# Performance work log

Hardware: AMD Instinct MI355X
Metric: run time of the kernel (lower is better)

The kernel has to match this reference:

```python
import jax, jax.numpy as jnp
import numpy as np

XYZ_MIN = jnp.array([-1.0, -1.0, -1.0], dtype=jnp.float32)
XYZ_MAX = jnp.array([1.0, 1.0, 1.0], dtype=jnp.float32)
ACT_SHIFT = float(np.log(1.0 / (1.0 - 1e-6) - 1.0))  # density bias shift
WS = 100  # world_size per axis for num_voxels=1024000 in [-1,1]^3
R, P = 4096, 128  # rays, points per ray


def grid_sample_3d(grid, xyz):
    """Trilinear grid_sample, align_corners=True, zeros padding.
    grid: [C, D, H, W] (D=z, H=y, W=x); xyz: [N, 3] world coords. Returns [N, C]."""
    C, D, H, W = grid.shape
    norm = (xyz - XYZ_MIN) / (XYZ_MAX - XYZ_MIN) * 2.0 - 1.0  # [-1,1]
    sizes = jnp.array([W, H, D], dtype=norm.dtype)
    pix = (norm + 1.0) * 0.5 * (sizes - 1.0)  # align_corners=True mapping
    p0f = jnp.floor(pix)
    frac = pix - p0f
    p0 = p0f.astype(jnp.int32)
    out = jnp.zeros((xyz.shape[0], C), dtype=grid.dtype)
    for dx in (0, 1):
        for dy in (0, 1):
            for dz in (0, 1):
                ix, iy, iz = p0[:, 0] + dx, p0[:, 1] + dy, p0[:, 2] + dz
                wx = frac[:, 0] if dx else 1.0 - frac[:, 0]
                wy = frac[:, 1] if dy else 1.0 - frac[:, 1]
                wz = frac[:, 2] if dz else 1.0 - frac[:, 2]
                valid = ((ix >= 0) & (ix < W) & (iy >= 0) & (iy < H)
                         & (iz >= 0) & (iz < D))
                ixc = jnp.clip(ix, 0, W - 1)
                iyc = jnp.clip(iy, 0, H - 1)
                izc = jnp.clip(iz, 0, D - 1)
                vals = grid[:, izc, iyc, ixc].T  # [N, C]
                out = out + vals * (wx * wy * wz * valid)[:, None]
    return out


def setup_inputs() -> dict:
    key = jax.random.key(0)
    ks = jax.random.split(key, 12)
    origins = jax.random.uniform(ks[0], (R, 3), jnp.float32, -0.5, 0.5)
    directions = jax.random.normal(ks[1], (R, 3), jnp.float32)
    lengths = jax.random.uniform(ks[2], (R, P), jnp.float32, 0.05, 0.6)
    grid_density = jax.random.normal(ks[3], (1, WS, WS, WS), jnp.float32) * 0.1
    grid_color = jax.random.normal(ks[4], (12, WS, WS, WS), jnp.float32) * 0.1
    d_in = 12 + 27
    w1 = jax.random.normal(ks[5], (d_in, 128), jnp.float32) / np.sqrt(d_in)
    b1 = jnp.zeros((128,), jnp.float32)
    w2 = jax.random.normal(ks[6], (128, 128), jnp.float32) / np.sqrt(128)
    b2 = jnp.zeros((128,), jnp.float32)
    w3 = jax.random.normal(ks[7], (128, 3), jnp.float32) / np.sqrt(128)
    b3 = jnp.zeros((3,), jnp.float32)
    return dict(origins=origins, directions=directions, lengths=lengths,
                grid_density=grid_density, grid_color=grid_color,
                w1=w1, b1=b1, w2=w2, b2=b2, w3=w3, b3=b3)


def reference(origins, directions, lengths, grid_density, grid_color,
              w1, b1, w2, b2, w3, b3):
    # ray points: [R, P, 3]
    pts = origins[:, None, :] + directions[:, None, :] * lengths[:, :, None]
    flat = pts.reshape(-1, 3)
    # density branch
    density = grid_sample_3d(grid_density, flat).reshape(R, P, 1)
    interval = jnp.linalg.norm(directions, axis=-1)[:, None, None]
    alpha = 1.0 - (1.0 + jnp.exp(density + ACT_SHIFT)) ** (-interval)
    # color branch: 12-ch feature grid + view-dir PE + small MLP
    color = grid_sample_3d(grid_color, flat).reshape(R, P, 12)
    freqs = jnp.array([1.0, 2.0, 4.0, 8.0], dtype=jnp.float32)
    emb = (directions[:, :, None] * freqs).reshape(R, 12)
    emb = jnp.concatenate([directions, jnp.sin(emb), jnp.cos(emb)], -1)  # [R,27]
    emb = jnp.broadcast_to(emb[:, None, :], (R, P, 27))
    h = jnp.concatenate([color, emb], -1)  # [R,P,39]
    h = jax.nn.relu(h @ w1 + b1)
    h = jax.nn.relu(h @ w2 + b2)
    rgb = jax.nn.sigmoid(h @ w3 + b3)
    return alpha, rgb
```

## Files before the change

### kernel.cpp

```cpp
#include <hip/hip_runtime.h>
#include <hip/hip_bf16.h>
#include <math.h>


typedef __bf16 bf16x4 __attribute__((ext_vector_type(4)));
typedef __bf16 bf16x8 __attribute__((ext_vector_type(8)));
typedef float  f32x4  __attribute__((ext_vector_type(4)));

#define ACT_SHIFT_F (-13.815509557964774f)

#define PACK_B  53248
#define FEAT_B  32053248
#define NEED_FULL 48830464ull
#define NEED_PACK 32053248ull

__global__ __launch_bounds__(256)
void dvgo_prep(const float* __restrict__ g_gd, const float* __restrict__ g_gc,
               const float* __restrict__ g_w1, const float* __restrict__ g_w2,
               const float* __restrict__ g_w3, bf16x8* __restrict__ pack,
               __bf16* __restrict__ wsb, int wbase)
{
    const int bid = blockIdx.x;
    if (bid < wbase) {
        const int gi = bid * 256 + threadIdx.x;
        if (gi >= 1000000) return;
        bf16x8 v0, v1;
        #pragma unroll
        for (int c = 0; c < 8; ++c) v0[c] = (__bf16)g_gc[c * 1000000 + gi];
        #pragma unroll
        for (int c = 0; c < 4; ++c) v1[c] = (__bf16)g_gc[(8 + c) * 1000000 + gi];
        v1[4] = (__bf16)g_gd[gi];
        v1[5] = (__bf16)0.0f; v1[6] = (__bf16)0.0f; v1[7] = (__bf16)0.0f;
        pack[gi * 2 + 0] = v0;
        pack[gi * 2 + 1] = v1;
        return;
    }
    const int idx = (bid - wbase) * 256 + threadIdx.x;
    if (idx < 8192) {
        const int j = idx & 7, lane = (idx >> 3) & 63, ks = (idx >> 9) & 1, ct = idx >> 10;
        const int n = ct * 16 + (lane & 15);
        const int k = ks * 32 + ((lane >> 4) & 3) * 8 + j;
        wsb[idx] = (__bf16)((k < 39) ? g_w1[k * 128 + n] : 0.0f);
    } else if (idx < 24576) {
        const int i2 = idx - 8192;
        const int j = i2 & 7, lane = (i2 >> 3) & 63, ks = (i2 >> 9) & 3, ct = i2 >> 11;
        const int n = ct * 16 + (lane & 15);
        const int k = ks * 32 + ((lane >> 4) & 3) * 8 + j;
        wsb[idx] = (__bf16)g_w2[k * 128 + n];
    } else if (idx < 26624) {
        const int i3 = idx - 24576;
        const int j = i3 & 7, lane = (i3 >> 3) & 63, ks = i3 >> 9;
        const int c = lane & 15;
        const int k = ks * 32 + ((lane >> 4) & 3) * 8 + j;
        wsb[idx] = (__bf16)((c < 3) ? g_w3[k * 3 + c] : 0.0f);
    }
}

__global__ __launch_bounds__(256, 6)
void dvgo_gather(const float* __restrict__ g_org, const float* __restrict__ g_dir,
                 const float* __restrict__ g_len, const bf16x8* __restrict__ pack,
                 __bf16* __restrict__ feat, float* __restrict__ out_alpha)
{
    const int pt  = blockIdx.x * 256 + threadIdx.x;
    const int ray = pt >> 7;
    const float d0 = g_dir[ray*3+0], d1 = g_dir[ray*3+1], d2 = g_dir[ray*3+2];
    const float o0 = g_org[ray*3+0], o1 = g_org[ray*3+1], o2 = g_org[ray*3+2];
    const float len = g_len[pt];

    const float px = (o0 + d0*len + 1.0f) * 49.5f;
    const float py = (o1 + d1*len + 1.0f) * 49.5f;
    const float pz = (o2 + d2*len + 1.0f) * 49.5f;
    const float fx = floorf(px), fy = floorf(py), fz = floorf(pz);
    const int ix = (int)fx, iy = (int)fy, iz = (int)fz;
    const float qx = px - fx, qy = py - fy, qz = pz - fz;
    const float wxa[2] = {1.0f - qx, qx};
    const float wya[2] = {1.0f - qy, qy};
    const float wza[2] = {1.0f - qz, qz};
    const int  cxa[2] = {min(max(ix,0),99),   min(max(ix+1,0),99)};
    const int  cya[2] = {min(max(iy,0),99),   min(max(iy+1,0),99)};
    const int  cza[2] = {min(max(iz,0),99),   min(max(iz+1,0),99)};
    const bool vxa[2] = {(unsigned)ix < 100u, (unsigned)(ix+1) < 100u};
    const bool vya[2] = {(unsigned)iy < 100u, (unsigned)(iy+1) < 100u};
    const bool vza[2] = {(unsigned)iz < 100u, (unsigned)(iz+1) < 100u};

    float den = 0.0f;
    float cc[12];
    #pragma unroll
    for (int c = 0; c < 12; ++c) cc[c] = 0.0f;

    #pragma unroll
    for (int dz = 0; dz < 2; ++dz)
    #pragma unroll
    for (int dy = 0; dy < 2; ++dy)
    #pragma unroll
    for (int dx = 0; dx < 2; ++dx) {
        float w = wxa[dx] * wya[dy] * wza[dz];
        if (!(vxa[dx] && vya[dy] && vza[dz])) w = 0.0f;
        const int gi = (cza[dz]*100 + cya[dy])*100 + cxa[dx];
        const bf16x8 v0 = pack[gi*2 + 0];
        const bf16x8 v1 = pack[gi*2 + 1];
        #pragma unroll
        for (int c = 0; c < 8; ++c) cc[c]     += w * (float)v0[c];
        #pragma unroll
        for (int c = 0; c < 4; ++c) cc[8 + c] += w * (float)v1[c];
        den += w * (float)v1[4];
    }

    const float interval = sqrtf(d0*d0 + d1*d1 + d2*d2);
    const float e = expf(den + ACT_SHIFT_F);
    out_alpha[pt] = -expm1f(-interval * log1pf(e));

    bf16x8 f0, f1;
    #pragma unroll
    for (int c = 0; c < 8; ++c) f0[c] = (__bf16)cc[c];
    #pragma unroll
    for (int c = 0; c < 4; ++c) f1[c] = (__bf16)cc[8 + c];
    f1[4] = (__bf16)d0; f1[5] = (__bf16)d1; f1[6] = (__bf16)d2;
    f1[7] = (__bf16)sinf(d0);
    bf16x8* fo = (bf16x8*)(feat + (size_t)pt * 16);
    fo[0] = f0;
    fo[1] = f1;
}

__global__ __launch_bounds__(256, 3)
void dvgo_mlp(const bf16x8* __restrict__ wf, const __bf16* __restrict__ feat,
              const float* __restrict__ g_dir,
              const float* __restrict__ g_b1, const float* __restrict__ g_b2,
              const float* __restrict__ g_b3, float* __restrict__ out_rgb)
{
    __shared__ __align__(16) char smem[32768];
    const int tid  = threadIdx.x;
    const int ray  = blockIdx.x;
    const int lane = tid & 63;
    const int wid  = tid >> 6;
    const int lr   = lane & 15;
    const int lk   = lane >> 4;

    const float d0 = g_dir[ray*3+0], d1 = g_dir[ray*3+1], d2 = g_dir[ray*3+2];

    const int kbase = (lk >= 2) ? lk * 8 : 32;
    bf16x8 eqv;
    #pragma unroll
    for (int j = 0; j < 8; ++j) {
        const int k = kbase + j;
        const bool is_sin = (k >= 16) && (k <= 26);
        const bool is_cos = (k >= 27) && (k <= 38);
        const int m = is_sin ? (k - 15) : (k - 27);
        const int mi = m >> 2;
        const float di = (mi == 0) ? d0 : ((mi == 1) ? d1 : d2);
        const float a = di * (float)(1 << (m & 3));
        float v = is_sin ? sinf(a) : cosf(a);
        if (!is_sin && !is_cos) v = 0.0f;
        eqv[j] = (__bf16)v;
    }
    bf16x8 zed;
    #pragma unroll
    for (int j = 0; j < 8; ++j) zed[j] = (__bf16)0.0f;
    const bf16x8 bq1 = (lk == 0) ? eqv : zed;

    bf16x8 ft[8];
    #pragma unroll
    for (int rt = 0; rt < 8; ++rt) {
        const int pt = ray*128 + rt*16 + lr;
        ft[rt] = *(const bf16x8*)(feat + (size_t)pt*16 + (lk >= 1 ? 8 : 0));
    }

    bf16x8 aw1[2][2];
    #pragma unroll
    for (int c2 = 0; c2 < 2; ++c2)
        #pragma unroll
        for (int ks = 0; ks < 2; ++ks)
            aw1[c2][ks] = wf[((wid*2 + c2)*2 + ks)*64 + lane];

    f32x4 acc1[8][2];
    #pragma unroll
    for (int rt = 0; rt < 8; ++rt)
        #pragma unroll
        for (int c2 = 0; c2 < 2; ++c2) acc1[rt][c2] = (f32x4){0.f,0.f,0.f,0.f};
    #pragma unroll
    for (int rt = 0; rt < 8; ++rt) {
        const bf16x8 b0 = (lk < 2) ? ft[rt] : eqv;
        #pragma unroll
        for (int c2 = 0; c2 < 2; ++c2) {
            acc1[rt][c2] = __builtin_amdgcn_mfma_f32_16x16x32_bf16(aw1[c2][0], b0,  acc1[rt][c2], 0, 0, 0);
            acc1[rt][c2] = __builtin_amdgcn_mfma_f32_16x16x32_bf16(aw1[c2][1], bq1, acc1[rt][c2], 0, 0, 0);
        }
    }

    bf16x8 aw2[2][4];
    #pragma unroll
    for (int c2 = 0; c2 < 2; ++c2)
        #pragma unroll
        for (int ks = 0; ks < 4; ++ks)
            aw2[c2][ks] = wf[1024 + ((wid*2 + c2)*4 + ks)*64 + lane];

    #pragma unroll
    for (int c2 = 0; c2 < 2; ++c2) {
        const int nb = (wid*2 + c2)*16 + lk*4;
        const f32x4 bv = *(const f32x4*)(g_b1 + nb);
        #pragma unroll
        for (int rt = 0; rt < 8; ++rt) {
            const int pt = rt*16 + lr;
            bf16x4 hv;
            #pragma unroll
            for (int r = 0; r < 4; ++r) hv[r] = (__bf16)fmaxf(acc1[rt][c2][r] + bv[r], 0.0f);
            const int a = (pt*256 + nb*2) ^ ((pt & 7) << 4);
            *(bf16x4*)(smem + a) = hv;
        }
    }
    __syncthreads();

    f32x4 acc2[8][2];
    #pragma unroll
    for (int rt = 0; rt < 8; ++rt)
        #pragma unroll
        for (int c2 = 0; c2 < 2; ++c2) acc2[rt][c2] = (f32x4){0.f,0.f,0.f,0.f};
    #pragma unroll
    for (int rt = 0; rt < 8; ++rt) {
        const int pt = rt*16 + lr;
        const int base = pt*256, sz = (pt & 7) << 4;
        bf16x8 hq[4];
        #pragma unroll
        for (int ks = 0; ks < 4; ++ks)
            hq[ks] = *(const bf16x8*)(smem + ((base + (ks*32 + lk*8)*2) ^ sz));
        #pragma unroll
        for (int c2 = 0; c2 < 2; ++c2)
            #pragma unroll
            for (int ks = 0; ks < 4; ++ks)
                acc2[rt][c2] = __builtin_amdgcn_mfma_f32_16x16x32_bf16(aw2[c2][ks], hq[ks], acc2[rt][c2], 0, 0, 0);
    }

    bf16x8 aw3[4];
    #pragma unroll
    for (int ks = 0; ks < 4; ++ks) aw3[ks] = wf[3072 + ks*64 + lane];

    __syncthreads();

    #pragma unroll
    for (int c2 = 0; c2 < 2; ++c2) {
        const int nb = (wid*2 + c2)*16 + lk*4;
        const f32x4 bv = *(const f32x4*)(g_b2 + nb);
        #pragma unroll
        for (int rt = 0; rt < 8; ++rt) {
            const int pt = rt*16 + lr;
            bf16x4 hv;
            #pragma unroll
            for (int r = 0; r < 4; ++r) hv[r] = (__bf16)fmaxf(acc2[rt][c2][r] + bv[r], 0.0f);
            const int a = (pt*256 + nb*2) ^ ((pt & 7) << 4);
            *(bf16x4*)(smem + a) = hv;
        }
    }
    __syncthreads();

    f32x4 acc3[2];
    acc3[0] = (f32x4){0.f,0.f,0.f,0.f};
    acc3[1] = (f32x4){0.f,0.f,0.f,0.f};
    #pragma unroll
    for (int q = 0; q < 2; ++q) {
        const int pt = (wid*2 + q)*16 + lr;
        const int base = pt*256, sz = (pt & 7) << 4;
        #pragma unroll
        for (int ks = 0; ks < 4; ++ks) {
            const bf16x8 hq = *(const bf16x8*)(smem + ((base + (ks*32 + lk*8)*2) ^ sz));
            acc3[q] = __builtin_amdgcn_mfma_f32_16x16x32_bf16(aw3[ks], hq, acc3[q], 0, 0, 0);
        }
    }
    if (lk == 0) {
        const float b30 = g_b3[0], b31 = g_b3[1], b32 = g_b3[2];
        #pragma unroll
        for (int q = 0; q < 2; ++q) {
            const int pt = ray*128 + (wid*2 + q)*16 + lr;
            out_rgb[pt*3 + 0] = 1.0f / (1.0f + expf(-(acc3[q][0] + b30)));
            out_rgb[pt*3 + 1] = 1.0f / (1.0f + expf(-(acc3[q][1] + b31)));
            out_rgb[pt*3 + 2] = 1.0f / (1.0f + expf(-(acc3[q][2] + b32)));
        }
    }
}

#define FB_FEAT_OFF 0
#define FB_PCC_OFF  16384
#define FB_H1_OFF   0
#define FB_PRGB_OFF 0

template <bool PACKED>
__global__ __launch_bounds__(256, 4)
void dvgo_main(const float* __restrict__ g_org, const float* __restrict__ g_dir,
               const float* __restrict__ g_len, const float* __restrict__ g_gd,
               const float* __restrict__ g_gc, const float* __restrict__ g_b1,
               const float* __restrict__ g_b2, const float* __restrict__ g_w3,
               const float* __restrict__ g_b3, const bf16x8* __restrict__ wf,
               const bf16x8* __restrict__ g_pack,
               float* __restrict__ out_alpha, float* __restrict__ out_rgb)
{
    __shared__ __align__(16) char smem[32768];
    float* smf = (float*)smem;
    const int tid = threadIdx.x;
    const int ray = blockIdx.x;
    const float d0 = g_dir[ray*3+0], d1 = g_dir[ray*3+1], d2 = g_dir[ray*3+2];
    {
        const float o0 = g_org[ray*3+0], o1 = g_org[ray*3+1], o2 = g_org[ray*3+2];
        const int p = tid & 127;
        const int dzv = tid >> 7;
        const float len = g_len[ray*128 + p];
        const float px = (o0 + d0*len + 1.0f) * 49.5f;
        const float py = (o1 + d1*len + 1.0f) * 49.5f;
        const float pz = (o2 + d2*len + 1.0f) * 49.5f;
        const float fx = floorf(px), fy = floorf(py), fz = floorf(pz);
        const int ix = (int)fx, iy = (int)fy, iz0 = (int)fz;
        const float qx = px - fx, qy = py - fy, qz = pz - fz;
        const float wxa[2] = {1.0f - qx, qx};
        const float wya[2] = {1.0f - qy, qy};
        const int  cxa[2] = {min(max(ix,0),99),   min(max(ix+1,0),99)};
        const int  cya[2] = {min(max(iy,0),99),   min(max(iy+1,0),99)};
        const bool vxa[2] = {(unsigned)ix < 100u, (unsigned)(ix+1) < 100u};
        const bool vya[2] = {(unsigned)iy < 100u, (unsigned)(iy+1) < 100u};
        const int  iz = iz0 + dzv;
        const float wz = dzv ? qz : (1.0f - qz);
        const int  cz = min(max(iz,0),99);
        const bool vz = (unsigned)iz < 100u;
        float den = 0.0f;
        float cc[12];
        #pragma unroll
        for (int c = 0; c < 12; ++c) cc[c] = 0.0f;
        #pragma unroll
        for (int dy = 0; dy < 2; ++dy)
        #pragma unroll
        for (int dx = 0; dx < 2; ++dx) {
            float w = wxa[dx] * wya[dy] * wz;
            if (!(vxa[dx] && vya[dy] && vz)) w = 0.0f;
            const int gi = (cz*100 + cya[dy])*100 + cxa[dx];
            if (PACKED) {
                const bf16x8 v0 = g_pack[gi*2 + 0];
                const bf16x8 v1 = g_pack[gi*2 + 1];
                #pragma unroll
                for (int c = 0; c < 8; ++c) cc[c]     += w * (float)v0[c];
                #pragma unroll
                for (int c = 0; c < 4; ++c) cc[8 + c] += w * (float)v1[c];
                den += w * (float)v1[4];
            } else {
                den += w * g_gd[gi];
                #pragma unroll
                for (int c = 0; c < 12; ++c) cc[c] += w * g_gc[c*1000000 + gi];
            }
        }
        if (dzv) {
            #pragma unroll
            for (int c = 0; c < 12; ++c) smf[FB_PCC_OFF/4 + p*13 + c] = cc[c];
            smf[FB_PCC_OFF/4 + p*13 + 12] = den;
        }
        __syncthreads();
        if (!dzv) {
            #pragma unroll
            for (int c = 0; c < 12; ++c) cc[c] += smf[FB_PCC_OFF/4 + p*13 + c];
            den += smf[FB_PCC_OFF/4 + p*13 + 12];
            const float interval = sqrtf(d0*d0 + d1*d1 + d2*d2);
            const float e = expf(den + ACT_SHIFT_F);
            out_alpha[ray*128 + p] = -expm1f(-interval * log1pf(e));
            bf16x8 f0; bf16x4 f1;
            #pragma unroll
            for (int c = 0; c < 8; ++c) f0[c] = (__bf16)cc[c];
            #pragma unroll
            for (int c = 0; c < 4; ++c) f1[c] = (__bf16)cc[8+c];
            const int swz = (p & 7) << 4;
            *reinterpret_cast<bf16x8*>(smem + ((FB_FEAT_OFF + p*128 +  0) ^ swz)) = f0;
            *reinterpret_cast<bf16x4*>(smem + ((FB_FEAT_OFF + p*128 + 16) ^ swz)) = f1;
        } else {
            float vals[52];
            vals[0] = d0; vals[1] = d1; vals[2] = d2;
            #pragma unroll
            for (int i = 0; i < 3; ++i) {
                const float di = (i == 0) ? d0 : ((i == 1) ? d1 : d2);
                #pragma unroll
                for (int j = 0; j < 4; ++j) {
                    const float a = di * (float)(1 << j);
                    vals[3  + i*4 + j] = sinf(a);
                    vals[15 + i*4 + j] = cosf(a);
                }
            }
            #pragma unroll
            for (int c = 27; c < 52; ++c) vals[c] = 0.0f;
            const int swz = (p & 7) << 4;
            #pragma unroll
            for (int i = 0; i < 13; ++i) {
                bf16x4 v4;
                #pragma unroll
                for (int r = 0; r < 4; ++r) v4[r] = (__bf16)vals[i*4 + r];
                *reinterpret_cast<bf16x4*>(smem + ((FB_FEAT_OFF + p*128 + 24 + i*8) ^ swz)) = v4;
            }
        }
    }
    __syncthreads();
    const int lane = tid & 63;
    const int wid  = tid >> 6;
    const int lr   = lane & 15;
    const int lk   = lane >> 4;
    {
        bf16x8 bf[2][2];
        #pragma unroll
        for (int rt = 0; rt < 2; ++rt)
            #pragma unroll
            for (int ks = 0; ks < 2; ++ks) {
                const int pt = wid*32 + rt*16 + lr;
                int a = FB_FEAT_OFF + pt*128 + ks*64 + lk*16; a ^= (pt & 7) << 4;
                bf[rt][ks] = *reinterpret_cast<const bf16x8*>(smem + a);
            }
        __syncthreads();
        f32x4 acc1[2][8];
        #pragma unroll
        for (int rt = 0; rt < 2; ++rt)
            #pragma unroll
            for (int ct = 0; ct < 8; ++ct) acc1[rt][ct] = (f32x4){0.f,0.f,0.f,0.f};
        #pragma unroll
        for (int ct = 0; ct < 8; ++ct) {
            const bf16x8 aw0 = wf[(ct*2 + 0)*64 + lane];
            const bf16x8 aw1 = wf[(ct*2 + 1)*64 + lane];
            #pragma unroll
            for (int rt = 0; rt < 2; ++rt) {
                acc1[rt][ct] = __builtin_amdgcn_mfma_f32_16x16x32_bf16(aw0, bf[rt][0], acc1[rt][ct], 0, 0, 0);
                acc1[rt][ct] = __builtin_amdgcn_mfma_f32_16x16x32_bf16(aw1, bf[rt][1], acc1[rt][ct], 0, 0, 0);
            }
        }
        #pragma unroll
        for (int ct = 0; ct < 8; ++ct) {
            const f32x4 b1v = *reinterpret_cast<const f32x4*>(g_b1 + ct*16 + lk*4);
            #pragma unroll
            for (int rt = 0; rt < 2; ++rt) {
                const int pt = wid*32 + rt*16 + lr;
                bf16x4 hv;
                #pragma unroll
                for (int r = 0; r < 4; ++r)
                    hv[r] = (__bf16)fmaxf(acc1[rt][ct][r] + b1v[r], 0.0f);
                int a = FB_H1_OFF + pt*256 + ct*32 + lk*8; a ^= (pt & 7) << 4;
                *reinterpret_cast<bf16x4*>(smem + a) = hv;
            }
        }
    }
    __syncthreads();
    const int wr = wid >> 1, wc = wid & 1;
    f32x4 acc2[4][4];
    #pragma unroll
    for (int rt = 0; rt < 4; ++rt)
        #pragma unroll
        for (int ct = 0; ct < 4; ++ct) acc2[rt][ct] = (f32x4){0.f,0.f,0.f,0.f};
    #pragma unroll
    for (int ks = 0; ks < 4; ++ks) {
        bf16x8 a2[4];
        #pragma unroll
        for (int rt = 0; rt < 4; ++rt) {
            const int pt = wr*64 + rt*16 + lr;
            int a = FB_H1_OFF + pt*256 + ks*64 + lk*16; a ^= (pt & 7) << 4;
            a2[rt] = *reinterpret_cast<const bf16x8*>(smem + a);
        }
        #pragma unroll
        for (int ct = 0; ct < 4; ++ct) {
            const int ctg = wc*4 + ct;
            const bf16x8 b2f = wf[1024 + (ctg*4 + ks)*64 + lane];
            #pragma unroll
            for (int rt = 0; rt < 4; ++rt)
                acc2[rt][ct] = __builtin_amdgcn_mfma_f32_16x16x32_bf16(a2[rt], b2f, acc2[rt][ct], 0, 0, 0);
        }
    }
    __syncthreads();
    {
        float b2v[4], w30[4], w31[4], w32[4];
        #pragma unroll
        for (int ct = 0; ct < 4; ++ct) {
            const int n2 = wc*64 + ct*16 + lr;
            b2v[ct] = g_b2[n2];
            w30[ct] = g_w3[n2*3 + 0];
            w31[ct] = g_w3[n2*3 + 1];
            w32[ct] = g_w3[n2*3 + 2];
        }
        #pragma unroll
        for (int rt = 0; rt < 4; ++rt)
            #pragma unroll
            for (int r = 0; r < 4; ++r) {
                float s0 = 0.f, s1 = 0.f, s2 = 0.f;
                #pragma unroll
                for (int ct = 0; ct < 4; ++ct) {
                    const float v = fmaxf(acc2[rt][ct][r] + b2v[ct], 0.0f);
                    s0 = fmaf(v, w30[ct], s0);
                    s1 = fmaf(v, w31[ct], s1);
                    s2 = fmaf(v, w32[ct], s2);
                }
                #pragma unroll
                for (int off = 1; off < 16; off <<= 1) {
                    s0 += __shfl_xor(s0, off);
                    s1 += __shfl_xor(s1, off);
                    s2 += __shfl_xor(s2, off);
                }
                if (lr == 0) {
                    const int pt = wr*64 + rt*16 + lk*4 + r;
                    const int base = FB_PRGB_OFF/4 + (wc*128 + pt)*3;
                    smf[base + 0] = s0;
                    smf[base + 1] = s1;
                    smf[base + 2] = s2;
                }
            }
    }
    __syncthreads();
    if (tid < 128) {
        const int p = tid;
        const float s0 = smf[p*3 + 0] + smf[(128 + p)*3 + 0] + g_b3[0];
        const float s1 = smf[p*3 + 1] + smf[(128 + p)*3 + 1] + g_b3[1];
        const float s2 = smf[p*3 + 2] + smf[(128 + p)*3 + 2] + g_b3[2];
        const int pt = ray*128 + p;
        out_rgb[pt*3 + 0] = 1.0f / (1.0f + expf(-s0));
        out_rgb[pt*3 + 1] = 1.0f / (1.0f + expf(-s1));
        out_rgb[pt*3 + 2] = 1.0f / (1.0f + expf(-s2));
    }
}

extern "C" void kernel_launch(void* const* d_in, const int* in_sizes, int n_in,
                              void* d_out, int out_size, void* d_ws, size_t ws_size,
                              hipStream_t stream)
{
    const float* g_org = (const float*)d_in[0];
    const float* g_dir = (const float*)d_in[1];
    const float* g_len = (const float*)d_in[2];
    const float* g_gd  = (const float*)d_in[3];
    const float* g_gc  = (const float*)d_in[4];
    const float* g_w1  = (const float*)d_in[5];
    const float* g_b1  = (const float*)d_in[6];
    const float* g_w2  = (const float*)d_in[7];
    const float* g_b2  = (const float*)d_in[8];
    const float* g_w3  = (const float*)d_in[9];
    const float* g_b3  = (const float*)d_in[10];
    float* out = (float*)d_out;

    __bf16* wsb = (__bf16*)d_ws;
    bf16x8* pack = (bf16x8*)((char*)d_ws + PACK_B);

    if (ws_size >= NEED_FULL) {
        __bf16* feat = (__bf16*)((char*)d_ws + FEAT_B);
        dvgo_prep<<<4011, 256, 0, stream>>>(g_gd, g_gc, g_w1, g_w2, g_w3,
                                            pack, wsb, 3907);
        dvgo_gather<<<2048, 256, 0, stream>>>(g_org, g_dir, g_len, pack, feat, out);
        dvgo_mlp<<<4096, 256, 0, stream>>>((const bf16x8*)wsb, feat, g_dir,
                                           g_b1, g_b2, g_b3, out + 4096*128);
    } else if (ws_size >= NEED_PACK) {
        dvgo_prep<<<4011, 256, 0, stream>>>(g_gd, g_gc, g_w1, g_w2, g_w3,
                                            pack, wsb, 3907);
        dvgo_main<true><<<4096, 256, 0, stream>>>(g_org, g_dir, g_len, g_gd, g_gc,
                                                  g_b1, g_b2, g_w3, g_b3,
                                                  (const bf16x8*)wsb, pack,
                                                  out, out + 4096*128);
    } else {
        dvgo_prep<<<104, 256, 0, stream>>>(g_gd, g_gc, g_w1, g_w2, g_w3,
                                           pack, wsb, 0);
        dvgo_main<false><<<4096, 256, 0, stream>>>(g_org, g_dir, g_len, g_gd, g_gc,
                                                   g_b1, g_b2, g_w3, g_b3,
                                                   (const bf16x8*)wsb, nullptr,
                                                   out, out + 4096*128);
    }
}
```

Measured before the change: 83.40 us.

## Precompute per-ray view embedding in prep and cut MLP register pressure

Per-ray sin/cos positional embeddings are now computed once per ray in the prep kernel and stored to workspace, so the MLP kernel loads them instead of evaluating trig per lane. The MLP kernel is restructured to process layer 1 in two halves and layer 2 per column tile, with bias loads and swizzled LDS addresses hoisted. This lowers live accumulators so launch bounds can go from 3 to 4 blocks per SM. It adds workspace, an extra global read per ray, and shifts the feature/embedding lane mapping.

```diff
diff --git a/kernel.cpp b/kernel.cpp
--- a/kernel.cpp
+++ b/kernel.cpp
@@ -9,16 +9,18 @@
 
 #define ACT_SHIFT_F (-13.815509557964774f)
 
-#define PACK_B  53248
-#define FEAT_B  32053248
-#define NEED_FULL 48830464ull
-#define NEED_PACK 32053248ull
+#define EMB_B   53248
+#define PACK_B  315392
+#define FEAT_B  32315392
+#define NEED_FULL 49092608ull
+#define NEED_PACK 32315392ull
 
 __global__ __launch_bounds__(256)
 void dvgo_prep(const float* __restrict__ g_gd, const float* __restrict__ g_gc,
                const float* __restrict__ g_w1, const float* __restrict__ g_w2,
-               const float* __restrict__ g_w3, bf16x8* __restrict__ pack,
-               __bf16* __restrict__ wsb, int wbase)
+               const float* __restrict__ g_w3, const float* __restrict__ g_dir,
+               bf16x8* __restrict__ pack, __bf16* __restrict__ wsb,
+               __bf16* __restrict__ emb, int wbase)
 {
     const int bid = blockIdx.x;
     if (bid < wbase) {
@@ -53,6 +55,28 @@
         const int c = lane & 15;
         const int k = ks * 32 + ((lane >> 4) & 3) * 8 + j;
         wsb[idx] = (__bf16)((c < 3) ? g_w3[k * 3 + c] : 0.0f);
+    } else if (idx < 30720) {
+        const int ray = idx - 26624;
+        const float d0 = g_dir[ray*3+0], d1 = g_dir[ray*3+1], d2 = g_dir[ray*3+2];
+        __bf16 e[32];
+        #pragma unroll
+        for (int s = 0; s < 32; ++s) e[s] = (__bf16)0.0f;
+        #pragma unroll
+        for (int m = 0; m < 12; ++m) {
+            const int i = m >> 2, j = m & 3;
+            const float di = (i == 0) ? d0 : ((i == 1) ? d1 : d2);
+            const float a = di * (float)(1 << j);
+            if (m >= 1) e[m - 1] = (__bf16)sinf(a);
+            e[11 + m] = (__bf16)cosf(a);
+        }
+        bf16x8* o = (bf16x8*)(emb + (size_t)ray * 32);
+        #pragma unroll
+        for (int q = 0; q < 4; ++q) {
+            bf16x8 v;
+            #pragma unroll
+            for (int j = 0; j < 8; ++j) v[j] = e[q*8 + j];
+            o[q] = v;
+        }
     }
 }
 
@@ -122,9 +146,9 @@
     fo[1] = f1;
 }
 
-__global__ __launch_bounds__(256, 3)
-void dvgo_mlp(const bf16x8* __restrict__ wf, const __bf16* __restrict__ feat,
-              const float* __restrict__ g_dir,
+__global__ __launch_bounds__(256, 4)
+void dvgo_mlp(const bf16x8* __restrict__ wf, const __bf16* __restrict__ emb,
+              const __bf16* __restrict__ feat,
               const float* __restrict__ g_b1, const float* __restrict__ g_b2,
               const float* __restrict__ g_b3, float* __restrict__ out_rgb)
 {
@@ -135,35 +159,31 @@
     const int wid  = tid >> 6;
     const int lr   = lane & 15;
     const int lk   = lane >> 4;
-
-    const float d0 = g_dir[ray*3+0], d1 = g_dir[ray*3+1], d2 = g_dir[ray*3+2];
-
-    const int kbase = (lk >= 2) ? lk * 8 : 32;
-    bf16x8 eqv;
-    #pragma unroll
-    for (int j = 0; j < 8; ++j) {
-        const int k = kbase + j;
-        const bool is_sin = (k >= 16) && (k <= 26);
-        const bool is_cos = (k >= 27) && (k <= 38);
-        const int m = is_sin ? (k - 15) : (k - 27);
-        const int mi = m >> 2;
-        const float di = (mi == 0) ? d0 : ((mi == 1) ? d1 : d2);
-        const float a = di * (float)(1 << (m & 3));
-        float v = is_sin ? sinf(a) : cosf(a);
-        if (!is_sin && !is_cos) v = 0.0f;
-        eqv[j] = (__bf16)v;
-    }
+    const int sz   = (lr & 7) << 4;
+
+    int rbase[4];
+    #pragma unroll
+    for (int ks = 0; ks < 4; ++ks)
+        rbase[ks] = lr*256 + ((ks*64 + lk*16) ^ sz);
+    int wbase[2];
+    #pragma unroll
+    for (int c2 = 0; c2 < 2; ++c2)
+        wbase[c2] = lr*256 + ((((wid*2 + c2)*32) + lk*8) ^ sz);
+
+    const bf16x8 ev = *(const bf16x8*)(emb + (size_t)ray*32 + (((lk + 2) & 3) * 8));
     bf16x8 zed;
     #pragma unroll
     for (int j = 0; j < 8; ++j) zed[j] = (__bf16)0.0f;
-    const bf16x8 bq1 = (lk == 0) ? eqv : zed;
-
-    bf16x8 ft[8];
-    #pragma unroll
-    for (int rt = 0; rt < 8; ++rt) {
-        const int pt = ray*128 + rt*16 + lr;
-        ft[rt] = *(const bf16x8*)(feat + (size_t)pt*16 + (lk >= 1 ? 8 : 0));
-    }
+    const bf16x8 bq1 = (lk < 2) ? ev : zed;
+
+    f32x4 b1v[2], b2v[2];
+    #pragma unroll
+    for (int c2 = 0; c2 < 2; ++c2) {
+        const int nb = (wid*2 + c2)*16 + lk*4;
+        b1v[c2] = *(const f32x4*)(g_b1 + nb);
+        b2v[c2] = *(const f32x4*)(g_b2 + nb);
+    }
+    const float b30 = g_b3[0], b31 = g_b3[1], b32 = g_b3[2];
 
     bf16x8 aw1[2][2];
     #pragma unroll
@@ -172,101 +192,96 @@
         for (int ks = 0; ks < 2; ++ks)
             aw1[c2][ks] = wf[((wid*2 + c2)*2 + ks)*64 + lane];
 
-    f32x4 acc1[8][2];
-    #pragma unroll
-    for (int rt = 0; rt < 8; ++rt)
-        #pragma unroll
-        for (int c2 = 0; c2 < 2; ++c2) acc1[rt][c2] = (f32x4){0.f,0.f,0.f,0.f};
-    #pragma unroll
-    for (int rt = 0; rt < 8; ++rt) {
-        const bf16x8 b0 = (lk < 2) ? ft[rt] : eqv;
-        #pragma unroll
-        for (int c2 = 0; c2 < 2; ++c2) {
-            acc1[rt][c2] = __builtin_amdgcn_mfma_f32_16x16x32_bf16(aw1[c2][0], b0,  acc1[rt][c2], 0, 0, 0);
-            acc1[rt][c2] = __builtin_amdgcn_mfma_f32_16x16x32_bf16(aw1[c2][1], bq1, acc1[rt][c2], 0, 0, 0);
-        }
-    }
-
-    bf16x8 aw2[2][4];
+    #pragma unroll
+    for (int h = 0; h < 2; ++h) {
+        bf16x8 ft[4];
+        #pragma unroll
+        for (int r4 = 0; r4 < 4; ++r4) {
+            const int pt = ray*128 + (h*4 + r4)*16 + lr;
+            ft[r4] = *(const bf16x8*)(feat + (size_t)pt*16 + (lk & 1)*8);
+        }
+        f32x4 acc1[4][2];
+        #pragma unroll
+        for (int r4 = 0; r4 < 4; ++r4)
+            #pragma unroll
+            for (int c2 = 0; c2 < 2; ++c2) acc1[r4][c2] = (f32x4){0.f,0.f,0.f,0.f};
+        #pragma unroll
+        for (int r4 = 0; r4 < 4; ++r4) {
+            const bf16x8 b0 = (lk < 2) ? ft[r4] : ev;
+            #pragma unroll
+            for (int c2 = 0; c2 < 2; ++c2) {
+                acc1[r4][c2] = __builtin_amdgcn_mfma_f32_16x16x32_bf16(aw1[c2][0], b0,  acc1[r4][c2], 0, 0, 0);
+                acc1[r4][c2] = __builtin_amdgcn_mfma_f32_16x16x32_bf16(aw1[c2][1], bq1, acc1[r4][c2], 0, 0, 0);
+            }
+        }
+        #pragma unroll
+        for (int c2 = 0; c2 < 2; ++c2)
+            #pragma unroll
+            for (int r4 = 0; r4 < 4; ++r4) {
+                bf16x4 hv;
+                #pragma unroll
+                for (int r = 0; r < 4; ++r)
+                    hv[r] = (__bf16)fmaxf(acc1[r4][c2][r] + b1v[c2][r], 0.0f);
+                *(bf16x4*)(smem + wbase[c2] + (h*4 + r4)*4096) = hv;
+            }
+    }
+    __syncthreads();
+
+    bf16x4 h2p[2][8];
+    #pragma unroll
+    for (int c2 = 0; c2 < 2; ++c2) {
+        bf16x8 aw2[4];
+        #pragma unroll
+        for (int ks = 0; ks < 4; ++ks)
+            aw2[ks] = wf[1024 + ((wid*2 + c2)*4 + ks)*64 + lane];
+        f32x4 acc2[8];
+        #pragma unroll
+        for (int rt = 0; rt < 8; ++rt) acc2[rt] = (f32x4){0.f,0.f,0.f,0.f};
+        #pragma unroll
+        for (int rt = 0; rt < 8; ++rt) {
+            bf16x8 hq[4];
+            #pragma unroll
+            for (int ks = 0; ks < 4; ++ks)
+                hq[ks] = *(const bf16x8*)(smem + rbase[ks] + rt*4096);
+            #pragma unroll
+            for (int ks = 0; ks < 4; ++ks)
+                acc2[rt] = __builtin_amdgcn_mfma_f32_16x16x32_bf16(aw2[ks], hq[ks], acc2[rt], 0, 0, 0);
+        }
+        #pragma unroll
+        for (int rt = 0; rt < 8; ++rt) {
+            bf16x4 hv;
+            #pragma unroll
+            for (int r = 0; r < 4; ++r)
+                hv[r] = (__bf16)fmaxf(acc2[rt][r] + b2v[c2][r], 0.0f);
+            h2p[c2][rt] = hv;
+        }
+    }
+
+    bf16x8 aw3[4];
+    #pragma unroll
+    for (int ks = 0; ks < 4; ++ks) aw3[ks] = wf[3072 + ks*64 + lane];
+
+    __syncthreads();
+
     #pragma unroll
     for (int c2 = 0; c2 < 2; ++c2)
         #pragma unroll
-        for (int ks = 0; ks < 4; ++ks)
-            aw2[c2][ks] = wf[1024 + ((wid*2 + c2)*4 + ks)*64 + lane];
-
-    #pragma unroll
-    for (int c2 = 0; c2 < 2; ++c2) {
-        const int nb = (wid*2 + c2)*16 + lk*4;
-        const f32x4 bv = *(const f32x4*)(g_b1 + nb);
-        #pragma unroll
-        for (int rt = 0; rt < 8; ++rt) {
-            const int pt = rt*16 + lr;
-            bf16x4 hv;
-            #pragma unroll
-            for (int r = 0; r < 4; ++r) hv[r] = (__bf16)fmaxf(acc1[rt][c2][r] + bv[r], 0.0f);
-            const int a = (pt*256 + nb*2) ^ ((pt & 7) << 4);
-            *(bf16x4*)(smem + a) = hv;
-        }
-    }
-    __syncthreads();
-
-    f32x4 acc2[8][2];
-    #pragma unroll
-    for (int rt = 0; rt < 8; ++rt)
-        #pragma unroll
-        for (int c2 = 0; c2 < 2; ++c2) acc2[rt][c2] = (f32x4){0.f,0.f,0.f,0.f};
-    #pragma unroll
-    for (int rt = 0; rt < 8; ++rt) {
-        const int pt = rt*16 + lr;
-        const int base = pt*256, sz = (pt & 7) << 4;
-        bf16x8 hq[4];
-        #pragma unroll
-        for (int ks = 0; ks < 4; ++ks)
-            hq[ks] = *(const bf16x8*)(smem + ((base + (ks*32 + lk*8)*2) ^ sz));
-        #pragma unroll
-        for (int c2 = 0; c2 < 2; ++c2)
-            #pragma unroll
-            for (int ks = 0; ks < 4; ++ks)
-                acc2[rt][c2] = __builtin_amdgcn_mfma_f32_16x16x32_bf16(aw2[c2][ks], hq[ks], acc2[rt][c2], 0, 0, 0);
-    }
-
-    bf16x8 aw3[4];
-    #pragma unroll
-    for (int ks = 0; ks < 4; ++ks) aw3[ks] = wf[3072 + ks*64 + lane];
-
-    __syncthreads();
-
-    #pragma unroll
-    for (int c2 = 0; c2 < 2; ++c2) {
-        const int nb = (wid*2 + c2)*16 + lk*4;
-        const f32x4 bv = *(const f32x4*)(g_b2 + nb);
-        #pragma unroll
-        for (int rt = 0; rt < 8; ++rt) {
-            const int pt = rt*16 + lr;
-            bf16x4 hv;
-            #pragma unroll
-            for (int r = 0; r < 4; ++r) hv[r] = (__bf16)fmaxf(acc2[rt][c2][r] + bv[r], 0.0f);
-            const int a = (pt*256 + nb*2) ^ ((pt & 7) << 4);
-            *(bf16x4*)(smem + a) = hv;
-        }
-    }
-    __syncthreads();
-
+        for (int rt = 0; rt < 8; ++rt)
+            *(bf16x4*)(smem + wbase[c2] + rt*4096) = h2p[c2][rt];
+    __syncthreads();
+
+    const int g3 = wid * 8192;
     f32x4 acc3[2];
     acc3[0] = (f32x4){0.f,0.f,0.f,0.f};
     acc3[1] = (f32x4){0.f,0.f,0.f,0.f};
     #pragma unroll
-    for (int q = 0; q < 2; ++q) {
-        const int pt = (wid*2 + q)*16 + lr;
-        const int base = pt*256, sz = (pt & 7) << 4;
+    for (int q = 0; q < 2; ++q)
         #pragma unroll
         for (int ks = 0; ks < 4; ++ks) {
-            const bf16x8 hq = *(const bf16x8*)(smem + ((base + (ks*32 + lk*8)*2) ^ sz));
+            const bf16x8 hq = *(const bf16x8*)(smem + rbase[ks] + g3 + q*4096);
             acc3[q] = __builtin_amdgcn_mfma_f32_16x16x32_bf16(aw3[ks], hq, acc3[q], 0, 0, 0);
         }
-    }
     if (lk == 0) {
-        const float b30 = g_b3[0], b31 = g_b3[1], b32 = g_b3[2];
         #pragma unroll
         for (int q = 0; q < 2; ++q) {
             const int pt = ray*128 + (wid*2 + q)*16 + lr;
@@ -528,26 +543,27 @@
     const float* g_b3  = (const float*)d_in[10];
     float* out = (float*)d_out;
 
-    __bf16* wsb = (__bf16*)d_ws;
+    __bf16* wsb  = (__bf16*)d_ws;
+    __bf16* emb  = (__bf16*)((char*)d_ws + EMB_B);
     bf16x8* pack = (bf16x8*)((char*)d_ws + PACK_B);
 
     if (ws_size >= NEED_FULL) {
         __bf16* feat = (__bf16*)((char*)d_ws + FEAT_B);
-        dvgo_prep<<<4011, 256, 0, stream>>>(g_gd, g_gc, g_w1, g_w2, g_w3,
-                                            pack, wsb, 3907);
+        dvgo_prep<<<4027, 256, 0, stream>>>(g_gd, g_gc, g_w1, g_w2, g_w3, g_dir,
+                                            pack, wsb, emb, 3907);
         dvgo_gather<<<2048, 256, 0, stream>>>(g_org, g_dir, g_len, pack, feat, out);
-        dvgo_mlp<<<4096, 256, 0, stream>>>((const bf16x8*)wsb, feat, g_dir,
+        dvgo_mlp<<<4096, 256, 0, stream>>>((const bf16x8*)wsb, emb, feat,
                                            g_b1, g_b2, g_b3, out + 4096*128);
     } else if (ws_size >= NEED_PACK) {
-        dvgo_prep<<<4011, 256, 0, stream>>>(g_gd, g_gc, g_w1, g_w2, g_w3,
-                                            pack, wsb, 3907);
+        dvgo_prep<<<4011, 256, 0, stream>>>(g_gd, g_gc, g_w1, g_w2, g_w3, g_dir,
+                                            pack, wsb, emb, 3907);
         dvgo_main<true><<<4096, 256, 0, stream>>>(g_org, g_dir, g_len, g_gd, g_gc,
                                                   g_b1, g_b2, g_w3, g_b3,
                                                   (const bf16x8*)wsb, pack,
                                                   out, out + 4096*128);
     } else {
-        dvgo_prep<<<104, 256, 0, stream>>>(g_gd, g_gc, g_w1, g_w2, g_w3,
-                                           pack, wsb, 0);
+        dvgo_prep<<<104, 256, 0, stream>>>(g_gd, g_gc, g_w1, g_w2, g_w3, g_dir,
+                                           pack, wsb, emb, 0);
         dvgo_main<false><<<4096, 256, 0, stream>>>(g_org, g_dir, g_len, g_gd, g_gc,
                                                    g_b1, g_b2, g_w3, g_b3,
                                                    (const bf16x8*)wsb, nullptr,
```

Result: slower. 135.2 us (+62.1%).
